# Optimization experiments

Hardware: AMD Instinct MI355X
Metric: run time of the kernel (lower is better)

The kernel has to match this reference:

```python
import jax, jax.numpy as jnp
import numpy as np

P, G, F, H = 128, 256, 1024, 512
EPS = 1e-5

def _bn(x, g, b, m, v):
    # eval-mode BatchNorm1d over last dim
    return (x - m) / jnp.sqrt(v + EPS) * g + b

def _lrelu(x):
    return jnp.where(x > 0, x, 0.1 * x)

def setup_inputs():
    key = jax.random.key(0)
    ks = iter(jax.random.split(key, 64))
    rn = lambda s, sc=1.0: jax.random.normal(next(ks), s, dtype=jnp.float32) * sc
    ru = lambda s: jax.random.uniform(next(ks), s, dtype=jnp.float32) + 0.5
    return {
        "f_p": rn((P, F)), "f_g": rn((G, F)),
        "bn_g": ru((F,)), "bn_b": rn((F,), 0.1), "bn_m": rn((F,), 0.1), "bn_v": ru((F,)),
        "rf_W1": rn((F, F), 0.02), "rf_b1": rn((F,), 0.01),
        "rf1_g": ru((F,)), "rf1_b": rn((F,), 0.1), "rf1_m": rn((F,), 0.1), "rf1_v": ru((F,)),
        "rf_W2": rn((F, F), 0.02), "rf_b2": rn((F,), 0.01),
        "rf2_g": ru((F,)), "rf2_b": rn((F,), 0.1), "rf2_m": rn((F,), 0.1), "rf2_v": ru((F,)),
        "sfc_W": rn((F, H), 0.02), "sfc_b": rn((H,), 0.01),
        "sbn_g": ru((H,)), "sbn_b": rn((H,), 0.1), "sbn_m": rn((H,), 0.1), "sbn_v": ru((H,)),
        "scl_W": rn((H, 1), 0.001), "scl_b": rn((1,), 0.001),
        "ffc_W": rn((F, H), 0.02), "ffc_b": rn((H,), 0.01),
        "fbn_g": ru((H,)), "fbn_b": rn((H,), 0.1), "fbn_m": rn((H,), 0.1), "fbn_v": ru((H,)),
        "cls_W": rn((H, 1), 0.001), "cls_b": rn((1,), 0.001),
    }

def reference(f_p, f_g, bn_g, bn_b, bn_m, bn_v,
              rf_W1, rf_b1, rf1_g, rf1_b, rf1_m, rf1_v,
              rf_W2, rf_b2, rf2_g, rf2_b, rf2_m, rf2_v,
              sfc_W, sfc_b, sbn_g, sbn_b, sbn_m, sbn_v, scl_W, scl_b,
              ffc_W, ffc_b, fbn_g, fbn_b, fbn_m, fbn_v, cls_W, cls_b):
    # Siamese difference feature for every probe-gallery pair: d [P,G,F]
    d = _bn((f_p[:, None, :] - f_g[None, :, :]) ** 2, bn_g, bn_b, bn_m, bn_v)
    h = _lrelu(_bn(d @ rf_W1 + rf_b1, rf1_g, rf1_b, rf1_m, rf1_v))
    t = _lrelu(_bn(h @ rf_W2 + rf_b2, rf2_g, rf2_b, rf2_m, rf2_v))
    # Gallery-gallery scalar affinities via Siamese FcBlock + ClassBlock: w [G,G]
    dg = _bn((f_g[:, None, :] - f_g[None, :, :]) ** 2, bn_g, bn_b, bn_m, bn_v)
    hg = _lrelu(_bn(dg @ sfc_W + sfc_b, sbn_g, sbn_b, sbn_m, sbn_v))
    w = (hg @ scl_W + scl_b)[..., 0]
    # Graph diffusion over the gallery axis: d_new = t @ w  [P,G,F]
    d_new = jnp.einsum('pgf,gh->phf', t, w)
    # Per-pair FC + classifier -> scalar score per (probe, gallery) pair
    feat = _lrelu(_bn(d_new @ ffc_W + ffc_b, fbn_g, fbn_b, fbn_m, fbn_v))
    result = (feat @ cls_W + cls_b)[..., 0]
    return result
```

## Files before the change

### kernel.cpp

```cpp
#include <hip/hip_runtime.h>


typedef __bf16 bf16;
typedef __attribute__((ext_vector_type(8))) __bf16 bf16x8;
typedef __attribute__((ext_vector_type(4))) float f32x4;

#define EPSV 1e-5f

__device__ __forceinline__ void async_load16(const bf16* g, bf16* l) {
    __builtin_amdgcn_global_load_lds(
        (const __attribute__((address_space(1))) void*)g,
        (__attribute__((address_space(3))) void*)l, 16, 0, 0);
}

__global__ __launch_bounds__(256) void prep_kernel(
    const float* __restrict__ g, const float* __restrict__ b,
    const float* __restrict__ m, const float* __restrict__ v,
    const float* __restrict__ bias, float* __restrict__ scale,
    float* __restrict__ offset, int n)
{
    int i = blockIdx.x * 256 + threadIdx.x;
    if (i >= n) return;
    float s = g[i] / sqrtf(v[i] + EPSV);
    float o = b[i] - m[i] * s;
    if (bias) o += bias[i] * s;
    scale[i] = s;
    offset[i] = o;
}

__global__ __launch_bounds__(256) void wtrans_kernel(
    const float* __restrict__ in, bf16* __restrict__ out, int K, int N)
{
    int k = blockIdx.x * 256 + threadIdx.x;
    int n = blockIdx.y;
    out[(size_t)n * K + k] = (bf16)in[(size_t)k * N + n];
}

__global__ __launch_bounds__(256) void wconv_kernel(
    const float* __restrict__ w_acc, const float* __restrict__ sclb,
    bf16* __restrict__ wT)
{
    int tid = blockIdx.x * 256 + threadIdx.x;
    int g2 = tid >> 8, g1 = tid & 255;
    int idx = ((g1 >> 4) <= (g2 >> 4)) ? (g1 * 256 + g2) : (g2 * 256 + g1);
    wT[tid] = (bf16)(w_acc[idx] + sclb[0]);
}

__global__ __launch_bounds__(256) void finout_kernel(
    const float* __restrict__ acc, const float* __restrict__ clsb,
    float* __restrict__ out)
{
    int i = blockIdx.x * 256 + threadIdx.x;
    out[i] = acc[i] + clsb[0];
}

__global__ __launch_bounds__(512) void gemm256(
    const bf16* __restrict__ A,
    const float* __restrict__ pairX, const float* __restrict__ pairY,
    const float* __restrict__ ps, const float* __restrict__ po,
    const bf16* __restrict__ BT,
    bf16* __restrict__ C,
    int K, int N, int rowOff,
    long long batchA, long long batchB, long long batchC,
    const float* __restrict__ scale, const float* __restrict__ offset,
    int lrelu,
    const float* __restrict__ fuseW, float* __restrict__ facc,
    long long faccStride)
{
    __shared__ bf16 As[256 * 64];
    __shared__ bf16 Bs[256 * 64];
    const int tid  = threadIdx.x;
    const int lane = tid & 63;
    const int wave = tid >> 6;
    const int wrow = wave >> 2, wcol = wave & 3;
    const int row0 = blockIdx.y * 256;
    const int col0 = blockIdx.x * 256;
    const int q = lane >> 4, l16 = lane & 15;
    const int z = blockIdx.z;

    const bf16* Ap = A + (size_t)z * (size_t)batchA;
    const bf16* Bp = BT + (size_t)z * (size_t)batchB;

    f32x4 acc[8][4];
#pragma unroll
    for (int mi = 0; mi < 8; ++mi)
#pragma unroll
        for (int ni = 0; ni < 4; ++ni)
#pragma unroll
            for (int e = 0; e < 4; ++e) acc[mi][ni][e] = 0.f;

    for (int kk = 0; kk < K; kk += 64) {
        if (pairX) {
#pragma unroll
            for (int t = 0; t < 4; ++t) {
                int c = tid + t * 512;
                int r = c >> 3, ch = c & 7;
                int gr = rowOff + row0 + r;
                const float* xp = pairX + (size_t)(gr >> 8) * K + kk + ch * 8;
                const float* yp = pairY + (size_t)(gr & 255) * K + kk + ch * 8;
                f32x4 x0 = *(const f32x4*)xp, x1 = *(const f32x4*)(xp + 4);
                f32x4 y0 = *(const f32x4*)yp, y1 = *(const f32x4*)(yp + 4);
                f32x4 sa = *(const f32x4*)(ps + kk + ch * 8);
                f32x4 sb = *(const f32x4*)(ps + kk + ch * 8 + 4);
                f32x4 oa = *(const f32x4*)(po + kk + ch * 8);
                f32x4 ob = *(const f32x4*)(po + kk + ch * 8 + 4);
                bf16x8 dv;
#pragma unroll
                for (int j = 0; j < 4; ++j) {
                    float d0 = x0[j] - y0[j];
                    float d1 = x1[j] - y1[j];
                    dv[j]     = (bf16)(d0 * d0 * sa[j] + oa[j]);
                    dv[j + 4] = (bf16)(d1 * d1 * sb[j] + ob[j]);
                }
                *(bf16x8*)&As[r * 64 + ((ch ^ (r & 7)) * 8)] = dv;
            }
        } else {
#pragma unroll
            for (int t = 0; t < 4; ++t) {
                int idx = t * 512 + tid;
                int r = idx >> 3, sch = idx & 7;
                int gch = sch ^ (r & 7);
                async_load16(Ap + (size_t)(row0 + r) * K + kk + gch * 8,
                             &As[idx * 8]);
            }
        }
#pragma unroll
        for (int t = 0; t < 4; ++t) {
            int idx = t * 512 + tid;
            int r = idx >> 3, sch = idx & 7;
            int gch = sch ^ (r & 7);
            async_load16(Bp + (size_t)(col0 + r) * K + kk + gch * 8,
                         &Bs[idx * 8]);
        }
        __syncthreads();

#pragma unroll
        for (int s = 0; s < 2; ++s) {
            bf16x8 af[8], bfr[4];
#pragma unroll
            for (int mi = 0; mi < 8; ++mi) {
                int r = wrow * 128 + mi * 16 + l16;
                af[mi] = *(const bf16x8*)&As[r * 64 + (((s * 4 + q) ^ (r & 7)) * 8)];
            }
#pragma unroll
            for (int ni = 0; ni < 4; ++ni) {
                int rc = wcol * 64 + ni * 16 + l16;
                bfr[ni] = *(const bf16x8*)&Bs[rc * 64 + (((s * 4 + q) ^ (rc & 7)) * 8)];
            }
#pragma unroll
            for (int mi = 0; mi < 8; ++mi)
#pragma unroll
                for (int ni = 0; ni < 4; ++ni)
                    acc[mi][ni] = __builtin_amdgcn_mfma_f32_16x16x32_bf16(
                        af[mi], bfr[ni], acc[mi][ni], 0, 0, 0);
        }
        __syncthreads();
    }

    if (fuseW) {
#pragma unroll
        for (int mi = 0; mi < 8; ++mi)
#pragma unroll
            for (int i = 0; i < 4; ++i) {
                float rs = 0.f;
#pragma unroll
                for (int ni = 0; ni < 4; ++ni) {
                    int cc = col0 + wcol * 64 + ni * 16 + l16;
                    float val = acc[mi][ni][i] * scale[cc] + offset[cc];
                    val = val > 0.f ? val : 0.1f * val;
                    rs += val * fuseW[cc];
                }
                rs += __shfl_xor(rs, 1, 64);
                rs += __shfl_xor(rs, 2, 64);
                rs += __shfl_xor(rs, 4, 64);
                rs += __shfl_xor(rs, 8, 64);
                if (l16 == 0) {
                    int r = row0 + wrow * 128 + mi * 16 + q * 4 + i;
                    atomicAdd(facc + (size_t)z * faccStride + r, rs);
                }
            }
        return;
    }
    bf16* Cp = C + (size_t)z * (size_t)batchC;
#pragma unroll
    for (int mi = 0; mi < 8; ++mi)
#pragma unroll
        for (int ni = 0; ni < 4; ++ni)
#pragma unroll
            for (int i = 0; i < 4; ++i) {
                int r = row0 + wrow * 128 + mi * 16 + q * 4 + i;
                int cc = col0 + wcol * 64 + ni * 16 + l16;
                float val = acc[mi][ni][i];
                if (scale) val = val * scale[cc] + offset[cc];
                if (lrelu) val = val > 0.f ? val : 0.1f * val;
                Cp[(size_t)r * N + cc] = (bf16)val;
            }
}

__global__ __launch_bounds__(512) void gemm_aff(
    const float* __restrict__ pairX,
    const float* __restrict__ ps, const float* __restrict__ po,
    const bf16* __restrict__ BT,
    int K,
    const float* __restrict__ scale, const float* __restrict__ offset,
    const float* __restrict__ sclW, float* __restrict__ w_acc)
{
    __shared__ bf16 As[256 * 64];
    __shared__ bf16 Bs[128 * 64];
    const int tid  = threadIdx.x;
    const int lane = tid & 63;
    const int wave = tid >> 6;
    const int wrow = wave >> 1, wcol = wave & 1;
    const int q = lane >> 4, l16 = lane & 15;
    const int col0 = blockIdx.x * 128;

    int ta = 0, rem = blockIdx.y;
    while (rem >= 16 - ta) { rem -= 16 - ta; ++ta; }
    const int tb = ta + rem;

    f32x4 acc[4][4];
#pragma unroll
    for (int mi = 0; mi < 4; ++mi)
#pragma unroll
        for (int ni = 0; ni < 4; ++ni)
#pragma unroll
            for (int e = 0; e < 4; ++e) acc[mi][ni][e] = 0.f;

    for (int kk = 0; kk < K; kk += 64) {
#pragma unroll
        for (int t = 0; t < 4; ++t) {
            int c = tid + t * 512;
            int r = c >> 3, ch = c & 7;
            int g1 = ta * 16 + (r >> 4), g2 = tb * 16 + (r & 15);
            const float* xp = pairX + (size_t)g1 * K + kk + ch * 8;
            const float* yp = pairX + (size_t)g2 * K + kk + ch * 8;
            f32x4 x0 = *(const f32x4*)xp, x1 = *(const f32x4*)(xp + 4);
            f32x4 y0 = *(const f32x4*)yp, y1 = *(const f32x4*)(yp + 4);
            f32x4 sa = *(const f32x4*)(ps + kk + ch * 8);
            f32x4 sb = *(const f32x4*)(ps + kk + ch * 8 + 4);
            f32x4 oa = *(const f32x4*)(po + kk + ch * 8);
            f32x4 ob = *(const f32x4*)(po + kk + ch * 8 + 4);
            bf16x8 dv;
#pragma unroll
            for (int j = 0; j < 4; ++j) {
                float d0 = x0[j] - y0[j];
                float d1 = x1[j] - y1[j];
                dv[j]     = (bf16)(d0 * d0 * sa[j] + oa[j]);
                dv[j + 4] = (bf16)(d1 * d1 * sb[j] + ob[j]);
            }
            *(bf16x8*)&As[r * 64 + ((ch ^ (r & 7)) * 8)] = dv;
        }
#pragma unroll
        for (int t = 0; t < 2; ++t) {
            int idx = t * 512 + tid;
            int r = idx >> 3, sch = idx & 7;
            int gch = sch ^ (r & 7);
            async_load16(BT + (size_t)(col0 + r) * K + kk + gch * 8,
                         &Bs[idx * 8]);
        }
        __syncthreads();

#pragma unroll
        for (int s = 0; s < 2; ++s) {
            bf16x8 af[4], bfr[4];
#pragma unroll
            for (int mi = 0; mi < 4; ++mi) {
                int r = wrow * 64 + mi * 16 + l16;
                af[mi] = *(const bf16x8*)&As[r * 64 + (((s * 4 + q) ^ (r & 7)) * 8)];
            }
#pragma unroll
            for (int ni = 0; ni < 4; ++ni) {
                int rc = wcol * 64 + ni * 16 + l16;
                bfr[ni] = *(const bf16x8*)&Bs[rc * 64 + (((s * 4 + q) ^ (rc & 7)) * 8)];
            }
#pragma unroll
            for (int mi = 0; mi < 4; ++mi)
#pragma unroll
                for (int ni = 0; ni < 4; ++ni)
                    acc[mi][ni] = __builtin_amdgcn_mfma_f32_16x16x32_bf16(
                        af[mi], bfr[ni], acc[mi][ni], 0, 0, 0);
        }
        __syncthreads();
    }

#pragma unroll
    for (int mi = 0; mi < 4; ++mi)
#pragma unroll
        for (int i = 0; i < 4; ++i) {
            float rs = 0.f;
#pragma unroll
            for (int ni = 0; ni < 4; ++ni) {
                int cc = col0 + wcol * 64 + ni * 16 + l16;
                float val = acc[mi][ni][i] * scale[cc] + offset[cc];
                val = val > 0.f ? val : 0.1f * val;
                rs += val * sclW[cc];
            }
            rs += __shfl_xor(rs, 1, 64);
            rs += __shfl_xor(rs, 2, 64);
            rs += __shfl_xor(rs, 4, 64);
            rs += __shfl_xor(rs, 8, 64);
            if (l16 == 0) {
                int r = wrow * 64 + mi * 16 + q * 4 + i;
                int g1 = ta * 16 + (r >> 4), g2 = tb * 16 + (r & 15);
                atomicAdd(w_acc + g1 * 256 + g2, rs);
            }
        }
}

extern "C" void kernel_launch(void* const* d_in, const int* in_sizes, int n_in,
                              void* d_out, int out_size, void* d_ws, size_t ws_size,
                              hipStream_t stream)
{
    const float* f_p   = (const float*)d_in[0];
    const float* f_g   = (const float*)d_in[1];
    const float* bn_g  = (const float*)d_in[2];
    const float* bn_b  = (const float*)d_in[3];
    const float* bn_m  = (const float*)d_in[4];
    const float* bn_v  = (const float*)d_in[5];
    const float* rf_W1 = (const float*)d_in[6];
    const float* rf_b1 = (const float*)d_in[7];
    const float* rf1_g = (const float*)d_in[8];
    const float* rf1_b = (const float*)d_in[9];
    const float* rf1_m = (const float*)d_in[10];
    const float* rf1_v = (const float*)d_in[11];
    const float* rf_W2 = (const float*)d_in[12];
    const float* rf_b2 = (const float*)d_in[13];
    const float* rf2_g = (const float*)d_in[14];
    const float* rf2_b = (const float*)d_in[15];
    const float* rf2_m = (const float*)d_in[16];
    const float* rf2_v = (const float*)d_in[17];
    const float* sfc_W = (const float*)d_in[18];
    const float* sfc_b = (const float*)d_in[19];
    const float* sbn_g = (const float*)d_in[20];
    const float* sbn_b = (const float*)d_in[21];
    const float* sbn_m = (const float*)d_in[22];
    const float* sbn_v = (const float*)d_in[23];
    const float* scl_W = (const float*)d_in[24];
    const float* scl_b = (const float*)d_in[25];
    const float* ffc_W = (const float*)d_in[26];
    const float* ffc_b = (const float*)d_in[27];
    const float* fbn_g = (const float*)d_in[28];
    const float* fbn_b = (const float*)d_in[29];
    const float* fbn_m = (const float*)d_in[30];
    const float* fbn_v = (const float*)d_in[31];
    const float* cls_W = (const float*)d_in[32];
    const float* cls_b = (const float*)d_in[33];

    const size_t MB = 1ull << 20;
    char* ws = (char*)d_ws;
    float* SC      = (float*)(ws);
    float *s0 = SC,        *o0 = SC + 1024;
    float *s1 = SC + 2048, *o1 = SC + 3072;
    float *s2 = SC + 4096, *o2 = SC + 5120;
    float *s3 = SC + 6144, *o3 = SC + 6656;
    float *s4 = SC + 7168, *o4 = SC + 7680;
    float* w_acc   = (float*)(ws + 65536);
    float* out_acc = (float*)(ws + 327680);
    bf16* wT       = (bf16*)(ws + 458752);
    bf16* W1T      = (bf16*)(ws + 1 * MB);
    bf16* W2T      = (bf16*)(ws + 3 * MB);
    bf16* sfcT     = (bf16*)(ws + 5 * MB);
    bf16* ffcT     = (bf16*)(ws + 6 * MB);

    int nc;
    if      (ws_size >= 170 * MB) nc = 1;
    else if (ws_size >= 90 * MB)  nc = 2;
    else                          nc = 4;
    const int pc = 128 / nc;
    const int R  = pc * 256;
    const size_t hbytes = (size_t)R * 1024 * 2;
    bf16* bufA = (bf16*)(ws + 8 * MB);
    bf16* bufB = (bf16*)(ws + 8 * MB + hbytes);
    bf16* bufC = (bf16*)(ws + 8 * MB + 2 * hbytes);

    prep_kernel<<<dim3(4), 256, 0, stream>>>(bn_g, bn_b, bn_m, bn_v, nullptr, s0, o0, 1024);
    prep_kernel<<<dim3(4), 256, 0, stream>>>(rf1_g, rf1_b, rf1_m, rf1_v, rf_b1, s1, o1, 1024);
    prep_kernel<<<dim3(4), 256, 0, stream>>>(rf2_g, rf2_b, rf2_m, rf2_v, rf_b2, s2, o2, 1024);
    prep_kernel<<<dim3(2), 256, 0, stream>>>(sbn_g, sbn_b, sbn_m, sbn_v, sfc_b, s3, o3, 512);
    prep_kernel<<<dim3(2), 256, 0, stream>>>(fbn_g, fbn_b, fbn_m, fbn_v, ffc_b, s4, o4, 512);

    wtrans_kernel<<<dim3(4, 1024), 256, 0, stream>>>(rf_W1, W1T, 1024, 1024);
    wtrans_kernel<<<dim3(4, 1024), 256, 0, stream>>>(rf_W2, W2T, 1024, 1024);
    wtrans_kernel<<<dim3(4, 512), 256, 0, stream>>>(sfc_W, sfcT, 1024, 512);
    wtrans_kernel<<<dim3(4, 512), 256, 0, stream>>>(ffc_W, ffcT, 1024, 512);

    hipMemsetAsync(ws + 65536, 0, 393216, stream);

    gemm_aff<<<dim3(4, 136), 512, 0, stream>>>(
        f_g, s0, o0, sfcT, 1024, s3, o3, scl_W, w_acc);
    wconv_kernel<<<dim3(256), 256, 0, stream>>>(w_acc, scl_b, wT);

    for (int ci = 0; ci < nc; ++ci) {
        gemm256<<<dim3(4, R / 256), 512, 0, stream>>>(
            nullptr, f_p, f_g, s0, o0, W1T, bufA, 1024, 1024, ci * R,
            0, 0, 0, s1, o1, 1, nullptr, nullptr, 0);
        gemm256<<<dim3(4, R / 256), 512, 0, stream>>>(
            bufA, nullptr, nullptr, nullptr, nullptr, W2T, bufB, 1024, 1024, 0,
            0, 0, 0, s2, o2, 1, nullptr, nullptr, 0);
        gemm256<<<dim3(1, 2, pc), 512, 0, stream>>>(
            ffcT, nullptr, nullptr, nullptr, nullptr, bufB, bufC, 1024, 256, 0,
            0, (long long)256 * 1024, (long long)512 * 256,
            nullptr, nullptr, 0, nullptr, nullptr, 0);
        gemm256<<<dim3(2, 1, pc), 512, 0, stream>>>(
            wT, nullptr, nullptr, nullptr, nullptr, bufC, nullptr, 256, 512, 0,
            0, (long long)512 * 256, 0,
            s4, o4, 1, cls_W, out_acc + (size_t)ci * pc * 256, 256);
    }
    finout_kernel<<<dim3(128), 256, 0, stream>>>(out_acc, cls_b, (float*)d_out);
}
```

Baseline: 569.2 us.

## Double-buffer LDS tiles in gemm256 to overlap loads with MFMA

Doubles the A and B shared-memory tiles and prefetches the next K-slice into the alternate buffer while the current slice feeds the MFMAs, cutting one barrier per iteration. The aim is to hide global-to-LDS latency behind compute. LDS use doubles to 128KB per block, which may limit occupancy. The pairX path does synchronous register loads and compute, so it overlaps less.

```diff
diff --git a/kernel.cpp b/kernel.cpp
--- a/kernel.cpp
+++ b/kernel.cpp
@@ -67,8 +67,8 @@
     const float* __restrict__ fuseW, float* __restrict__ facc,
     long long faccStride)
 {
-    __shared__ bf16 As[256 * 64];
-    __shared__ bf16 Bs[256 * 64];
+    __shared__ bf16 As[2 * 256 * 64];
+    __shared__ bf16 Bs[2 * 256 * 64];
     const int tid  = threadIdx.x;
     const int lane = tid & 63;
     const int wave = tid >> 6;
@@ -89,7 +89,17 @@
 #pragma unroll
             for (int e = 0; e < 4; ++e) acc[mi][ni][e] = 0.f;
 
-    for (int kk = 0; kk < K; kk += 64) {
+    auto stageB = [&](int kk, bf16* dst) {
+#pragma unroll
+        for (int t = 0; t < 4; ++t) {
+            int idx = t * 512 + tid;
+            int r = idx >> 3, sch = idx & 7;
+            int gch = sch ^ (r & 7);
+            async_load16(Bp + (size_t)(col0 + r) * K + kk + gch * 8,
+                         &dst[idx * 8]);
+        }
+    };
+    auto stageA = [&](int kk, bf16* dst) {
         if (pairX) {
 #pragma unroll
             for (int t = 0; t < 4; ++t) {
@@ -112,7 +122,7 @@
                     dv[j]     = (bf16)(d0 * d0 * sa[j] + oa[j]);
                     dv[j + 4] = (bf16)(d1 * d1 * sb[j] + ob[j]);
                 }
-                *(bf16x8*)&As[r * 64 + ((ch ^ (r & 7)) * 8)] = dv;
+                *(bf16x8*)&dst[r * 64 + ((ch ^ (r & 7)) * 8)] = dv;
             }
         } else {
 #pragma unroll
@@ -121,31 +131,36 @@
                 int r = idx >> 3, sch = idx & 7;
                 int gch = sch ^ (r & 7);
                 async_load16(Ap + (size_t)(row0 + r) * K + kk + gch * 8,
-                             &As[idx * 8]);
-            }
-        }
-#pragma unroll
-        for (int t = 0; t < 4; ++t) {
-            int idx = t * 512 + tid;
-            int r = idx >> 3, sch = idx & 7;
-            int gch = sch ^ (r & 7);
-            async_load16(Bp + (size_t)(col0 + r) * K + kk + gch * 8,
-                         &Bs[idx * 8]);
-        }
-        __syncthreads();
-
+                             &dst[idx * 8]);
+            }
+        }
+    };
+
+    stageB(0, Bs);
+    stageA(0, As);
+    __syncthreads();
+
+    int cur = 0;
+    for (int kk = 0; kk < K; kk += 64) {
+        const bool pf = (kk + 64) < K;
+        if (pf) {
+            stageB(kk + 64, Bs + (cur ^ 1) * 16384);
+            stageA(kk + 64, As + (cur ^ 1) * 16384);
+        }
+        const bf16* Asb = As + cur * 16384;
+        const bf16* Bsb = Bs + cur * 16384;
 #pragma unroll
         for (int s = 0; s < 2; ++s) {
             bf16x8 af[8], bfr[4];
 #pragma unroll
             for (int mi = 0; mi < 8; ++mi) {
                 int r = wrow * 128 + mi * 16 + l16;
-                af[mi] = *(const bf16x8*)&As[r * 64 + (((s * 4 + q) ^ (r & 7)) * 8)];
+                af[mi] = *(const bf16x8*)&Asb[r * 64 + (((s * 4 + q) ^ (r & 7)) * 8)];
             }
 #pragma unroll
             for (int ni = 0; ni < 4; ++ni) {
                 int rc = wcol * 64 + ni * 16 + l16;
-                bfr[ni] = *(const bf16x8*)&Bs[rc * 64 + (((s * 4 + q) ^ (rc & 7)) * 8)];
+                bfr[ni] = *(const bf16x8*)&Bsb[rc * 64 + (((s * 4 + q) ^ (rc & 7)) * 8)];
             }
 #pragma unroll
             for (int mi = 0; mi < 8; ++mi)
@@ -154,7 +169,10 @@
                     acc[mi][ni] = __builtin_amdgcn_mfma_f32_16x16x32_bf16(
                         af[mi], bfr[ni], acc[mi][ni], 0, 0, 0);
         }
-        __syncthreads();
+        if (pf) {
+            __syncthreads();
+            cur ^= 1;
+        }
     }
 
     if (fuseW) {
```

Result: no change. 560.9 us (-1.5%).
